# Performance work log

Hardware: AMD Instinct MI355X
Metric: run time of the kernel (lower is better)

The kernel has to match this reference:

```python
import jax, jax.numpy as jnp
import numpy as np

B, S, D_MODEL = 2, 2048, 512
N_HEADS, D_KV = 8, 64
NUM_BUCKETS, MAX_DISTANCE = 32, 128


def _relative_position_bucket(relative_position, num_buckets=NUM_BUCKETS, max_distance=MAX_DISTANCE):
    # bidirectional (is_decoder=False) bucketing, exactly as HF T5
    num_buckets = num_buckets // 2
    buckets = (relative_position > 0).astype(jnp.int32) * num_buckets
    rel = jnp.abs(relative_position)
    max_exact = num_buckets // 2
    is_small = rel < max_exact
    rel_f = jnp.maximum(rel, 1).astype(jnp.float32)
    val_if_large = max_exact + (
        jnp.log(rel_f / max_exact) / np.log(max_distance / max_exact) * (num_buckets - max_exact)
    ).astype(jnp.int32)
    val_if_large = jnp.minimum(val_if_large, num_buckets - 1)
    return buckets + jnp.where(is_small, rel, val_if_large)


def _compute_bias(rel_bias_emb, q_len, k_len):
    ctx = jnp.arange(q_len)[:, None]          # [q,1]
    mem = jnp.arange(k_len)[None, :]          # [1,k]
    buckets = _relative_position_bucket(mem - ctx)        # [q,k] int32
    bias = rel_bias_emb[buckets]                           # [q,k,H]
    return jnp.transpose(bias, (2, 0, 1))[None]            # [1,H,q,k]


def setup_inputs() -> dict:
    key = jax.random.key(0)
    ks = jax.random.split(key, 6)
    sc = 1.0 / np.sqrt(D_MODEL)
    return {
        "hidden_states": jax.random.normal(ks[0], (B, S, D_MODEL), jnp.float32),
        "Wq": jax.random.normal(ks[1], (D_MODEL, N_HEADS * D_KV), jnp.float32) * sc,
        "Wk": jax.random.normal(ks[2], (D_MODEL, N_HEADS * D_KV), jnp.float32) * sc,
        "Wv": jax.random.normal(ks[3], (D_MODEL, N_HEADS * D_KV), jnp.float32) * sc,
        "Wo": jax.random.normal(ks[4], (N_HEADS * D_KV, D_MODEL), jnp.float32) * sc,
        "rel_bias_emb": jax.random.normal(ks[5], (NUM_BUCKETS, N_HEADS), jnp.float32),
    }


def reference(hidden_states, Wq, Wk, Wv, Wo, rel_bias_emb):
    b, s, _ = hidden_states.shape

    def proj(W):  # [b,s,D] @ [D,H*Dk] -> [b,H,s,Dk]
        return (hidden_states @ W).reshape(b, s, N_HEADS, D_KV).transpose(0, 2, 1, 3)

    q = proj(Wq)
    k = proj(Wk)
    v = proj(Wv)

    # T5 attention: NO 1/sqrt(d) scaling
    scores = jnp.einsum("bhqd,bhkd->bhqk", q, k)
    position_bias = _compute_bias(rel_bias_emb, s, s)      # [1,H,s,s]
    scores = scores + position_bias
    attn = jax.nn.softmax(scores.astype(jnp.float32), axis=-1).astype(scores.dtype)
    # dropout p=0.0 in eval mode -> identity
    out = jnp.einsum("bhqk,bhkd->bhqd", attn, v)           # [b,H,s,Dk]
    out = out.transpose(0, 2, 1, 3).reshape(b, s, N_HEADS * D_KV)
    attn_output = out @ Wo                                  # [b,s,D]
    return attn_output, position_bias
```

## Files before the change

kernel.cpp:

```cpp
#include <hip/hip_runtime.h>

typedef __attribute__((ext_vector_type(8))) short short8;
typedef __attribute__((ext_vector_type(4))) float f32x4;
typedef __attribute__((ext_vector_type(16))) float f32x16;
typedef __attribute__((ext_vector_type(4))) float float4v;
typedef __attribute__((ext_vector_type(8))) float f32x8;
typedef __attribute__((ext_vector_type(4))) unsigned short us4;
typedef __attribute__((ext_vector_type(8))) unsigned short us8v;
typedef __attribute__((ext_vector_type(4))) unsigned int uint4v;

#define DEVI __device__ __forceinline__
#define MFMA16(a,b,c) __builtin_amdgcn_mfma_f32_16x16x32_bf16((a),(b),(c),0,0,0)
#define MFMA32(a,b,c) __builtin_amdgcn_mfma_f32_32x32x16_bf16((a),(b),(c),0,0,0)

DEVI unsigned short f2bf(float x) {
    unsigned u = __builtin_bit_cast(unsigned, x);
    u += 0x7FFFu + ((u >> 16) & 1u);
    return (unsigned short)(u >> 16);
}
DEVI float bf2f(unsigned short b) {
    return __builtin_bit_cast(float, ((unsigned)b) << 16);
}
DEVI unsigned cvt_pk_bf16(float lo, float hi) {
    unsigned r;
    asm("v_cvt_pk_bf16_f32 %0, %1, %2" : "=v"(r) : "v"(lo), "v"(hi));
    return r;
}

__global__ __launch_bounds__(256) void k_prep_hidden(const float* __restrict__ hid,
                                                     unsigned short* __restrict__ hh,
                                                     unsigned short* __restrict__ hl) {
    __shared__ float tile[64][65];
    const int bid = blockIdx.x;
    const int rt = bid >> 3, ct = bid & 7;
    const int t = threadIdx.x;
    const int r = t >> 2, cc = (t & 3) << 4;
    const float* sp = hid + (long)(rt * 64 + r) * 512 + ct * 64 + cc;
    #pragma unroll
    for (int j = 0; j < 16; j += 4) {
        float4v v = *reinterpret_cast<const float4v*>(sp + j);
        tile[r][cc + j + 0] = v[0];
        tile[r][cc + j + 1] = v[1];
        tile[r][cc + j + 2] = v[2];
        tile[r][cc + j + 3] = v[3];
    }
    __syncthreads();
    #pragma unroll
    for (int s = 0; s < 2; ++s) {
        int slot = t * 2 + s;
        int lane = slot & 63, i = (slot >> 6) & 3, ktl = slot >> 8;
        int ri = i * 16 + (lane & 15);
        int kc = ktl * 32 + (lane >> 4) * 8;
        us8v hv, lv;
        #pragma unroll
        for (int j = 0; j < 8; ++j) {
            float x = tile[ri][kc + j];
            unsigned short hb = f2bf(x);
            hv[j] = hb; lv[j] = f2bf(x - bf2f(hb));
        }
        long o = ((long)(rt * 16 + ct * 2 + ktl) * 4 + i) * 512 + lane * 8;
        *reinterpret_cast<us8v*>(hh + o) = hv;
        *reinterpret_cast<us8v*>(hl + o) = lv;
    }
}

__global__ __launch_bounds__(256) void k_prep_w(const float* __restrict__ wq, const float* __restrict__ wk,
                                                const float* __restrict__ wvp, const float* __restrict__ wo,
                                                unsigned short* __restrict__ wqthi, unsigned short* __restrict__ wqtlo,
                                                unsigned short* __restrict__ wkthi, unsigned short* __restrict__ wktlo,
                                                unsigned short* __restrict__ wvt, unsigned short* __restrict__ wot) {
    __shared__ float tile[64][65];
    const int bid = blockIdx.x;
    const int mat = bid >> 6, t6 = bid & 63;
    const int tr = t6 >> 3, tc = t6 & 7;
    const float* src = mat == 0 ? wq : mat == 1 ? wk : mat == 2 ? wvp : wo;
    const int t = threadIdx.x;
    const int r = t >> 2, cc = (t & 3) << 4;
    const float* sp = src + (long)(tr * 64 + r) * 512 + tc * 64 + cc;
    #pragma unroll
    for (int j = 0; j < 16; j += 4) {
        float4v v = *reinterpret_cast<const float4v*>(sp + j);
        tile[r][cc + j + 0] = v[0];
        tile[r][cc + j + 1] = v[1];
        tile[r][cc + j + 2] = v[2];
        tile[r][cc + j + 3] = v[3];
    }
    __syncthreads();
    us8v h0, h1, l0, l1;
    #pragma unroll
    for (int j = 0; j < 8; ++j) {
        float x = tile[cc + j][r];
        unsigned short hb = f2bf(x);
        h0[j] = hb; l0[j] = f2bf(x - bf2f(hb));
        float y = tile[cc + 8 + j][r];
        unsigned short hb2 = f2bf(y);
        h1[j] = hb2; l1[j] = f2bf(y - bf2f(hb2));
    }
    const int jj = r >> 4, li = r & 15;
    const int kt = (tr * 64 + cc) >> 5;
    const int g0 = (cc >> 3) & 3;
    const long bse = ((long)((tc * 16 + kt) * 4 + jj)) * 512;
    const long o0 = bse + (g0 * 16 + li) * 8;
    const long o1 = bse + ((g0 + 1) * 16 + li) * 8;
    if (mat <= 1) {
        unsigned short* oh = mat ? wkthi : wqthi;
        unsigned short* ol = mat ? wktlo : wqtlo;
        *reinterpret_cast<us8v*>(oh + o0) = h0;
        *reinterpret_cast<us8v*>(oh + o1) = h1;
        *reinterpret_cast<us8v*>(ol + o0) = l0;
        *reinterpret_cast<us8v*>(ol + o1) = l1;
    } else {
        unsigned short* oh = mat == 2 ? wvt : wot;
        *reinterpret_cast<us8v*>(oh + o0) = h0;
        *reinterpret_cast<us8v*>(oh + o1) = h1;
    }
}

DEVI int bucket_large(int a) {
    if (a < 12) return 8;
    if (a < 16) return 9;
    if (a < 23) return 10;
    if (a < 32) return 11;
    if (a < 46) return 12;
    if (a < 64) return 13;
    if (a < 91) return 14;
    return 15;
}
__global__ __launch_bounds__(256) void k_prep_bias(const float* __restrict__ emb, float* __restrict__ biasT) {
    int t = blockIdx.x * 256 + threadIdx.x;
    if (t >= 8 * 4095) return;
    int h = t / 4095;
    int idx = t - h * 4095;
    int rel = idx - 2047;
    int a = rel < 0 ? -rel : rel;
    int bucket = (rel > 0 ? 16 : 0) + (a < 8 ? a : bucket_large(a));
    biasT[h * 4096 + idx] = emb[bucket * 8 + h];
}

__global__ __launch_bounds__(256) void k_proj(const unsigned short* __restrict__ hh,
                                              const unsigned short* __restrict__ hl,
                                              const unsigned short* __restrict__ wqthi, const unsigned short* __restrict__ wqtlo,
                                              const unsigned short* __restrict__ wkthi, const unsigned short* __restrict__ wktlo,
                                              const unsigned short* __restrict__ wvt,
                                              unsigned short* __restrict__ q_hi, unsigned short* __restrict__ q_lo,
                                              unsigned short* __restrict__ ktiles,
                                              unsigned short* __restrict__ vtiles) {
    const int wgid = (blockIdx.x & 7) * 48 + (blockIdx.x >> 3);
    const int nt = wgid % 12, mt = wgid / 12;
    const int sec = nt >> 2;
    const bool isv = (sec == 2);
    const int tid = threadIdx.x, wv = tid >> 6, lane = tid & 63;
    const int wr = wv >> 1, wc = wv & 1;
    const int g = lane >> 4, li = lane & 15;
    const int m0 = mt * 128 + wr * 64;
    const int n0 = (nt & 3) * 128 + wc * 64;
    const unsigned short* bh_ = (sec == 0) ? wqthi : (sec == 1) ? wkthi : wvt;
    const unsigned short* bl_ = (sec == 0) ? wqtlo : wktlo;
    const int rt2 = m0 >> 6;
    const int ntile = n0 >> 6;

    f32x4 zf = {0.f, 0.f, 0.f, 0.f};
    f32x4 acc[4][4];
    #pragma unroll
    for (int i = 0; i < 4; ++i)
        #pragma unroll
        for (int j = 0; j < 4; ++j) acc[i][j] = zf;

    for (int ks = 0; ks < 512; ks += 32) {
        const int kt = ks >> 5;
        const long abase = ((long)(rt2 * 16 + kt) * 4) * 512 + lane * 8;
        const long bbase = ((long)(ntile * 16 + kt) * 4) * 512 + lane * 8;
        short8 ah[4], al[4], bhf[4], blf[4];
        #pragma unroll
        for (int i = 0; i < 4; ++i) {
            ah[i] = *reinterpret_cast<const short8*>(hh + abase + i * 512);
            if (!isv) al[i] = *reinterpret_cast<const short8*>(hl + abase + i * 512);
            bhf[i] = *reinterpret_cast<const short8*>(bh_ + bbase + i * 512);
            if (!isv) blf[i] = *reinterpret_cast<const short8*>(bl_ + bbase + i * 512);
        }
        #pragma unroll
        for (int i = 0; i < 4; ++i)
            #pragma unroll
            for (int j = 0; j < 4; ++j) {
                acc[i][j] = MFMA16(ah[i], bhf[j], acc[i][j]);
                if (!isv) {
                    acc[i][j] = MFMA16(ah[i], blf[j], acc[i][j]);
                    acc[i][j] = MFMA16(al[i], bhf[j], acc[i][j]);
                }
            }
    }

    if (sec == 0) {
        #pragma unroll
        for (int i = 0; i < 4; ++i) {
            int rowb = m0 + i * 16 + g * 4;
            #pragma unroll
            for (int j = 0; j < 4; ++j) {
                int col = n0 + j * 16 + li;
                #pragma unroll
                for (int r = 0; r < 4; ++r) {
                    float x = acc[i][j][r];
                    unsigned short hb = f2bf(x);
                    long o = (long)(rowb + r) * 512 + col;
                    q_hi[o] = hb;
                    q_lo[o] = f2bf(x - bf2f(hb));
                }
            }
        }
    } else if (sec == 1) {
        #pragma unroll
        for (int i = 0; i < 4; ++i) {
            int rowb = m0 + i * 16 + g * 4;
            #pragma unroll
            for (int j = 0; j < 4; ++j) {
                int col = n0 + j * 16 + li;
                int h2 = col >> 6, d = col & 63;
                int ds2 = d >> 4, j2 = d & 7, lhalf = (d >> 3) & 1;
                #pragma unroll
                for (int r = 0; r < 4; ++r) {
                    int srow = rowb + r;
                    int bloc = srow >> 11, k = srow & 2047;
                    long base = (long)((bloc * 8 + h2) * 64 + (k >> 5)) * 4096
                              + (((k & 31) | (lhalf << 5)) * 8 + j2);
                    float x = acc[i][j][r];
                    unsigned short hb = f2bf(x);
                    ktiles[base + ds2 * 512] = hb;
                    ktiles[base + (4 + ds2) * 512] = f2bf(x - bf2f(hb));
                }
            }
        }
    } else {
        #pragma unroll
        for (int i = 0; i < 4; ++i) {
            int rowb = m0 + i * 16 + g * 4;
            int bloc = rowb >> 11, k = rowb & 2047;
            int kt = k >> 5, t = (k >> 4) & 1, lhalf = (k >> 3) & 1, j0 = k & 7;
            #pragma unroll
            for (int j = 0; j < 4; ++j) {
                int col = n0 + j * 16 + li;
                int h2 = col >> 6, d = col & 63;
                int dblk = d >> 5;
                us4 w;
                #pragma unroll
                for (int r = 0; r < 4; ++r) w[r] = f2bf(acc[i][j][r]);
                long off2 = (long)((bloc * 8 + h2) * 64 + kt) * 2048
                          + (dblk * 2 + t) * 512 + (((d & 31) | (lhalf << 5)) * 8 + j0);
                *reinterpret_cast<us4*>(vtiles + off2) = w;
            }
        }
    }
}

__global__ __launch_bounds__(128) void k_attn(const unsigned short* __restrict__ qhi,
                                              const unsigned short* __restrict__ qlo,
                                              const unsigned short* __restrict__ ktiles,
                                              const unsigned short* __restrict__ vtiles,
                                              const float* __restrict__ biasT,
                                              unsigned short* __restrict__ ctx,
                                              float* __restrict__ outb) {
    __shared__ float lb[2080];
    __shared__ float mrg[64][34];
    const int xcd = blockIdx.x & 7, lidx = blockIdx.x >> 3;
    const int bh = ((lidx >> 6) << 3) | xcd;
    const int qt = lidx & 63;
    const int b = bh >> 3, h = bh & 7;
    const int tid = threadIdx.x;
    const int kh = tid >> 6, lane = tid & 63;
    const int ql_ = lane & 31, hi = lane >> 5;
    const int q0 = qt * 32;

    for (int i = tid; i < 2080; i += 128) lb[i] = biasT[h * 4096 + (2016 - q0) + i];
    __syncthreads();

    const int q = q0 + ql_;
    const long rowQ = (long)(b * 2048 + q) * 512 + h * 64 + hi * 8;
    short8 qfh[4], qfl[4];
    #pragma unroll
    for (int ds = 0; ds < 4; ++ds) {
        qfh[ds] = *reinterpret_cast<const short8*>(qhi + rowQ + ds * 16);
        qfl[ds] = *reinterpret_cast<const short8*>(qlo + rowQ + ds * 16);
    }
    const int kbeg = kh * 1024;
    const unsigned short* ktb = ktiles + ((long)bh * 64 + (kbeg >> 5)) * 4096;
    const unsigned short* vtb = vtiles + ((long)bh * 64 + (kbeg >> 5)) * 2048;

    f32x16 o0, o1;
    #pragma unroll
    for (int i = 0; i < 16; ++i) { o0[i] = 0.f; o1[i] = 0.f; }
    float m_run = -__builtin_inff(), l_run = 0.f;

    short8 kAh[4], kAl[4], kBh[4], kBl[4], vA[4], vB[4];
    #pragma unroll
    for (int ds = 0; ds < 4; ++ds) {
        kAh[ds] = *reinterpret_cast<const short8*>(ktb + ds * 512 + lane * 8);
        kAl[ds] = *reinterpret_cast<const short8*>(ktb + (4 + ds) * 512 + lane * 8);
    }
    #pragma unroll
    for (int i = 0; i < 4; ++i)
        vA[i] = *reinterpret_cast<const short8*>(vtb + i * 512 + lane * 8);

    auto step = [&](short8 (&ckh)[4], short8 (&ckl)[4], short8 (&cv)[4],
                    short8 (&nkh)[4], short8 (&nkl)[4], short8 (&nv)[4], int it) {
        f32x16 ssA, ssB;
        #pragma unroll
        for (int i = 0; i < 16; ++i) { ssA[i] = 0.f; ssB[i] = 0.f; }
        __builtin_amdgcn_s_setprio(1);
        #pragma unroll
        for (int ds = 0; ds < 4; ++ds) {
            ssA = MFMA32(ckh[ds], qfh[ds], ssA);
            ssB = MFMA32(ckh[ds], qfl[ds], ssB);
        }
        #pragma unroll
        for (int ds = 0; ds < 4; ++ds)
            ssA = MFMA32(ckl[ds], qfh[ds], ssA);
        __builtin_amdgcn_s_setprio(0);
        const long ko = (it + 1 < 32) ? (long)(it + 1) * 4096 : (long)it * 4096;
        const long vo = (it + 1 < 32) ? (long)(it + 1) * 2048 : (long)it * 2048;
        #pragma unroll
        for (int ds = 0; ds < 4; ++ds) {
            nkh[ds] = *reinterpret_cast<const short8*>(ktb + ko + ds * 512 + lane * 8);
            nkl[ds] = *reinterpret_cast<const short8*>(ktb + ko + (4 + ds) * 512 + lane * 8);
        }
        #pragma unroll
        for (int i = 0; i < 4; ++i)
            nv[i] = *reinterpret_cast<const short8*>(vtb + vo + i * 512 + lane * 8);
        const int k0 = kbeg + it * 32;
        const int ib = k0 - ql_ + 31 + 4 * hi;
        float s[16];
        #pragma unroll
        for (int r = 0; r < 16; ++r)
            s[r] = (ssA[r] + ssB[r]) + lb[ib + (r & 3) + 8 * (r >> 2)];
        float t0 = fmaxf(s[0], s[1]), t1 = fmaxf(s[2], s[3]), t2 = fmaxf(s[4], s[5]), t3 = fmaxf(s[6], s[7]);
        float t4 = fmaxf(s[8], s[9]), t5 = fmaxf(s[10], s[11]), t6 = fmaxf(s[12], s[13]), t7 = fmaxf(s[14], s[15]);
        float u0 = fmaxf(t0, t1), u1 = fmaxf(t2, t3), u2 = fmaxf(t4, t5), u3 = fmaxf(t6, t7);
        float mx = fmaxf(fmaxf(u0, u1), fmaxf(u2, u3));
        mx = fmaxf(mx, __shfl_xor(mx, 32));
        bool grown = mx > m_run;
        float mnew = fmaxf(m_run, mx);
        float scale = __expf(m_run - mnew);
        float p[16];
        #pragma unroll
        for (int r = 0; r < 16; ++r) p[r] = __expf(s[r] - mnew);
        unsigned W[8];
        float ps[8];
        #pragma unroll
        for (int r2 = 0; r2 < 8; ++r2) {
            unsigned w = cvt_pk_bf16(p[2 * r2], p[2 * r2 + 1]);
            W[r2] = w;
            float plo = __builtin_bit_cast(float, w << 16);
            float phi = __builtin_bit_cast(float, w & 0xFFFF0000u);
            ps[r2] = plo + phi;
        }
        float psum = ((ps[0] + ps[1]) + (ps[2] + ps[3])) + ((ps[4] + ps[5]) + (ps[6] + ps[7]));
        l_run = l_run * scale + psum;
        m_run = mnew;
        if (__any(grown)) {
            #pragma unroll
            for (int i = 0; i < 16; ++i) { o0[i] *= scale; o1[i] *= scale; }
        }
        unsigned Sw[8];
        #pragma unroll
        for (int r2 = 0; r2 < 8; ++r2) Sw[r2] = __shfl_xor(W[r2], 32);
        __builtin_amdgcn_s_setprio(1);
        #pragma unroll
        for (int t = 0; t < 2; ++t) {
            uint4v bw;
            bw[0] = hi ? Sw[4 * t + 2] : W[4 * t + 0];
            bw[1] = hi ? Sw[4 * t + 3] : W[4 * t + 1];
            bw[2] = hi ? W[4 * t + 2] : Sw[4 * t + 0];
            bw[3] = hi ? W[4 * t + 3] : Sw[4 * t + 1];
            short8 pf = __builtin_bit_cast(short8, bw);
            o0 = MFMA32(cv[t], pf, o0);
            o1 = MFMA32(cv[2 + t], pf, o1);
        }
        __builtin_amdgcn_s_setprio(0);
    };

    for (int it2 = 0; it2 < 32; it2 += 2) {
        step(kAh, kAl, vA, kBh, kBl, vB, it2);
        step(kBh, kBl, vB, kAh, kAl, vA, it2 + 1);
    }

    if (kh == 1) {
        float* mp = &mrg[lane][0];
        mp[0] = m_run; mp[1] = l_run;
        #pragma unroll
        for (int i = 0; i < 16; ++i) { mp[2 + i] = o0[i]; mp[18 + i] = o1[i]; }
    }
    __syncthreads();
    if (kh == 0) {
        const float* mp = &mrg[lane][0];
        float m2 = mp[0], l2 = mp[1];
        float ms = fmaxf(m_run, m2);
        float a1 = __expf(m_run - ms);
        float a2 = __expf(m2 - ms);
        float lt = l_run * a1 + l2 * a2;
        lt += __shfl_xor(lt, 32);
        float inv = 1.0f / lt;
        const int rt = b * 32 + (q >> 6), ii = (q >> 4) & 3, li2 = q & 15;
        const long baseA = ((long)(rt * 16 + 2 * h) * 4 + ii) * 512 + li2 * 8 + 4 * hi;
        #pragma unroll
        for (int a = 0; a < 4; ++a) {
            us4 w0, w1;
            #pragma unroll
            for (int c = 0; c < 4; ++c) {
                w0[c] = f2bf((o0[4 * a + c] * a1 + mp[2 + 4 * a + c] * a2) * inv);
                w1[c] = f2bf((o1[4 * a + c] * a1 + mp[18 + 4 * a + c] * a2) * inv);
            }
            *reinterpret_cast<us4*>(ctx + baseA + a * 128) = w0;
            *reinterpret_cast<us4*>(ctx + baseA + 2048 + a * 128) = w1;
        }
    }

    if (b == 0) {
        float* ob = outb + ((long)h * 2048 + q0) * 2048;
        const float* bsrc = biasT + h * 4096 + 2047 - q0;
        #pragma unroll 4
        for (int c = 0; c < 64; ++c) {
            int chunk = c * 128 + tid;
            int r = chunk >> 8;
            int k8 = (chunk & 255) * 8;
            const float* src = bsrc + (k8 - r);
            f32x8 w;
            #pragma unroll
            for (int i = 0; i < 8; ++i) w[i] = src[i];
            *reinterpret_cast<f32x8*>(ob + (long)r * 2048 + k8) = w;
        }
    }
}

__global__ __launch_bounds__(256) void k_oproj(const unsigned short* __restrict__ ctx,
                                               const unsigned short* __restrict__ wot,
                                               float* __restrict__ outp) {
    const int wgid = blockIdx.x;
    const int nt = wgid & 3, mt = wgid >> 2;
    const int tid = threadIdx.x, wv = tid >> 6, lane = tid & 63;
    const int wr = wv >> 1, wc = wv & 1;
    const int g = lane >> 4, li = lane & 15;
    const int m0 = mt * 128 + wr * 64;
    const int n0 = nt * 128 + wc * 64;
    const int rt2 = m0 >> 6, ntile = n0 >> 6;

    f32x4 zf = {0.f, 0.f, 0.f, 0.f};
    f32x4 acc[4][4];
    #pragma unroll
    for (int i = 0; i < 4; ++i)
        #pragma unroll
        for (int j = 0; j < 4; ++j) acc[i][j] = zf;

    for (int ks = 0; ks < 512; ks += 32) {
        const int kt = ks >> 5;
        const long abase = (long)(rt2 * 16 + kt) * 2048 + lane * 8;
        const long bbase = (long)(ntile * 16 + kt) * 2048 + lane * 8;
        short8 af[4], bf[4];
        #pragma unroll
        for (int i = 0; i < 4; ++i) {
            af[i] = *reinterpret_cast<const short8*>(ctx + abase + i * 512);
            bf[i] = *reinterpret_cast<const short8*>(wot + bbase + i * 512);
        }
        #pragma unroll
        for (int i = 0; i < 4; ++i)
            #pragma unroll
            for (int j = 0; j < 4; ++j)
                acc[i][j] = MFMA16(af[i], bf[j], acc[i][j]);
    }
    #pragma unroll
    for (int i = 0; i < 4; ++i) {
        int rowb = m0 + i * 16 + g * 4;
        #pragma unroll
        for (int j = 0; j < 4; ++j) {
            int col = n0 + j * 16 + li;
            #pragma unroll
            for (int r = 0; r < 4; ++r)
                outp[(long)(rowb + r) * 512 + col] = acc[i][j][r];
        }
    }
}

extern "C" void kernel_launch(void* const* d_in, const int* in_sizes, int n_in,
                              void* d_out, int out_size, void* d_ws, size_t ws_size,
                              hipStream_t stream) {
    const float* hidden = (const float*)d_in[0];
    const float* Wq = (const float*)d_in[1];
    const float* Wk = (const float*)d_in[2];
    const float* Wv = (const float*)d_in[3];
    const float* Wo = (const float*)d_in[4];
    const float* emb = (const float*)d_in[5];
    float* out = (float*)d_out;

    char* ws = (char*)d_ws;
    size_t off = 0;
    auto alloc = [&](size_t bytes) { char* p = ws + off; off += (bytes + 255) & ~(size_t)255; return p; };

    unsigned short* hid_hi = (unsigned short*)alloc(4096ull * 512 * 2);
    unsigned short* hid_lo = (unsigned short*)alloc(4096ull * 512 * 2);
    unsigned short* wqthi  = (unsigned short*)alloc(512ull * 512 * 2);
    unsigned short* wqtlo  = (unsigned short*)alloc(512ull * 512 * 2);
    unsigned short* wkthi  = (unsigned short*)alloc(512ull * 512 * 2);
    unsigned short* wktlo  = (unsigned short*)alloc(512ull * 512 * 2);
    unsigned short* wvt    = (unsigned short*)alloc(512ull * 512 * 2);
    unsigned short* wot    = (unsigned short*)alloc(512ull * 512 * 2);
    float*          biasT  = (float*)alloc(8ull * 4096 * 4);
    unsigned short* q_hi   = (unsigned short*)alloc(4096ull * 512 * 2);
    unsigned short* q_lo   = (unsigned short*)alloc(4096ull * 512 * 2);
    unsigned short* ktiles = (unsigned short*)alloc(16ull * 64 * 8 * 512 * 2);
    unsigned short* vtiles = (unsigned short*)alloc(16ull * 64 * 4 * 512 * 2);
    unsigned short* ctx    = (unsigned short*)alloc(4096ull * 512 * 2);

    k_prep_hidden<<<512, 256, 0, stream>>>(hidden, hid_hi, hid_lo);
    k_prep_w<<<256, 256, 0, stream>>>(Wq, Wk, Wv, Wo, wqthi, wqtlo, wkthi, wktlo, wvt, wot);
    k_prep_bias<<<128, 256, 0, stream>>>(emb, biasT);
    k_proj<<<384, 256, 0, stream>>>(hid_hi, hid_lo, wqthi, wqtlo, wkthi, wktlo, wvt,
                                    q_hi, q_lo, ktiles, vtiles);
    k_attn<<<1024, 128, 0, stream>>>(q_hi, q_lo, ktiles, vtiles, biasT, ctx, out + 2097152);
    k_oproj<<<128, 256, 0, stream>>>(ctx, wot, out);
}
```

Baseline: 127.6 us.

## Split attention key range across four waves per block with LDS merge

The attention kernel now launches 256 threads per block and splits the 2048 keys across four waves of 512 keys each instead of two waves of 1024. The three extra partial softmax states are merged through shared memory by wave 0. The row-sum is now taken from fp32 probabilities rather than bf16-rounded ones, and the max reduction is reshaped. The goal is more parallelism per query tile and shorter serial loops, at the cost of more LDS, a longer merge step and possibly lower occupancy.

Result: slower. 148.8 us (+16.6%).

```diff
diff --git a/kernel.cpp b/kernel.cpp
--- a/kernel.cpp
+++ b/kernel.cpp
@@ -251,7 +251,7 @@
     }
 }
 
-__global__ __launch_bounds__(128) void k_attn(const unsigned short* __restrict__ qhi,
+__global__ __launch_bounds__(256) void k_attn(const unsigned short* __restrict__ qhi,
                                               const unsigned short* __restrict__ qlo,
                                               const unsigned short* __restrict__ ktiles,
                                               const unsigned short* __restrict__ vtiles,
@@ -259,17 +259,17 @@
                                               unsigned short* __restrict__ ctx,
                                               float* __restrict__ outb) {
     __shared__ float lb[2080];
-    __shared__ float mrg[64][34];
+    __shared__ float mrg[3][64][34];
     const int xcd = blockIdx.x & 7, lidx = blockIdx.x >> 3;
     const int bh = ((lidx >> 6) << 3) | xcd;
     const int qt = lidx & 63;
     const int b = bh >> 3, h = bh & 7;
     const int tid = threadIdx.x;
-    const int kh = tid >> 6, lane = tid & 63;
+    const int kq = tid >> 6, lane = tid & 63;
     const int ql_ = lane & 31, hi = lane >> 5;
     const int q0 = qt * 32;
 
-    for (int i = tid; i < 2080; i += 128) lb[i] = biasT[h * 4096 + (2016 - q0) + i];
+    for (int i = tid; i < 2080; i += 256) lb[i] = biasT[h * 4096 + (2016 - q0) + i];
     __syncthreads();
 
     const int q = q0 + ql_;
@@ -280,7 +280,7 @@
         qfh[ds] = *reinterpret_cast<const short8*>(qhi + rowQ + ds * 16);
         qfl[ds] = *reinterpret_cast<const short8*>(qlo + rowQ + ds * 16);
     }
-    const int kbeg = kh * 1024;
+    const int kbeg = kq * 512;
     const unsigned short* ktb = ktiles + ((long)bh * 64 + (kbeg >> 5)) * 4096;
     const unsigned short* vtb = vtiles + ((long)bh * 64 + (kbeg >> 5)) * 2048;
 
@@ -314,8 +314,8 @@
         for (int ds = 0; ds < 4; ++ds)
             ssA = MFMA32(ckl[ds], qfh[ds], ssA);
         __builtin_amdgcn_s_setprio(0);
-        const long ko = (it + 1 < 32) ? (long)(it + 1) * 4096 : (long)it * 4096;
-        const long vo = (it + 1 < 32) ? (long)(it + 1) * 2048 : (long)it * 2048;
+        const long ko = (it + 1 < 16) ? (long)(it + 1) * 4096 : (long)it * 4096;
+        const long vo = (it + 1 < 16) ? (long)(it + 1) * 2048 : (long)it * 2048;
         #pragma unroll
         for (int ds = 0; ds < 4; ++ds) {
             nkh[ds] = *reinterpret_cast<const short8*>(ktb + ko + ds * 512 + lane * 8);
@@ -330,10 +330,14 @@
         #pragma unroll
         for (int r = 0; r < 16; ++r)
             s[r] = (ssA[r] + ssB[r]) + lb[ib + (r & 3) + 8 * (r >> 2)];
-        float t0 = fmaxf(s[0], s[1]), t1 = fmaxf(s[2], s[3]), t2 = fmaxf(s[4], s[5]), t3 = fmaxf(s[6], s[7]);
-        float t4 = fmaxf(s[8], s[9]), t5 = fmaxf(s[10], s[11]), t6 = fmaxf(s[12], s[13]), t7 = fmaxf(s[14], s[15]);
-        float u0 = fmaxf(t0, t1), u1 = fmaxf(t2, t3), u2 = fmaxf(t4, t5), u3 = fmaxf(t6, t7);
-        float mx = fmaxf(fmaxf(u0, u1), fmaxf(u2, u3));
+        float a0 = fmaxf(fmaxf(s[0], s[1]), s[2]);
+        float a1b = fmaxf(fmaxf(s[3], s[4]), s[5]);
+        float a2b = fmaxf(fmaxf(s[6], s[7]), s[8]);
+        float a3 = fmaxf(fmaxf(s[9], s[10]), s[11]);
+        float a4 = fmaxf(fmaxf(s[12], s[13]), s[14]);
+        float b0 = fmaxf(fmaxf(a0, a1b), a2b);
+        float b1 = fmaxf(fmaxf(a3, a4), s[15]);
+        float mx = fmaxf(b0, b1);
         mx = fmaxf(mx, __shfl_xor(mx, 32));
         bool grown = mx > m_run;
         float mnew = fmaxf(m_run, mx);
@@ -341,17 +345,12 @@
         float p[16];
         #pragma unroll
         for (int r = 0; r < 16; ++r) p[r] = __expf(s[r] - mnew);
+        float psum = (((p[0] + p[1]) + (p[2] + p[3])) + ((p[4] + p[5]) + (p[6] + p[7])))
+                   + (((p[8] + p[9]) + (p[10] + p[11])) + ((p[12] + p[13]) + (p[14] + p[15])));
         unsigned W[8];
-        float ps[8];
-        #pragma unroll
-        for (int r2 = 0; r2 < 8; ++r2) {
-            unsigned w = cvt_pk_bf16(p[2 * r2], p[2 * r2 + 1]);
-            W[r2] = w;
-            float plo = __builtin_bit_cast(float, w << 16);
-            float phi = __builtin_bit_cast(float, w & 0xFFFF0000u);
-            ps[r2] = plo + phi;
-        }
-        float psum = ((ps[0] + ps[1]) + (ps[2] + ps[3])) + ((ps[4] + ps[5]) + (ps[6] + ps[7]));
+        #pragma unroll
+        for (int r2 = 0; r2 < 8; ++r2)
+            W[r2] = cvt_pk_bf16(p[2 * r2], p[2 * r2 + 1]);
         l_run = l_run * scale + psum;
         m_run = mnew;
         if (__any(grown)) {
@@ -376,26 +375,35 @@
         __builtin_amdgcn_s_setprio(0);
     };
 
-    for (int it2 = 0; it2 < 32; it2 += 2) {
+    for (int it2 = 0; it2 < 16; it2 += 2) {
         step(kAh, kAl, vA, kBh, kBl, vB, it2);
         step(kBh, kBl, vB, kAh, kAl, vA, it2 + 1);
     }
 
-    if (kh == 1) {
-        float* mp = &mrg[lane][0];
+    if (kq != 0) {
+        float* mp = &mrg[kq - 1][lane][0];
         mp[0] = m_run; mp[1] = l_run;
         #pragma unroll
         for (int i = 0; i < 16; ++i) { mp[2 + i] = o0[i]; mp[18 + i] = o1[i]; }
     }
     __syncthreads();
-    if (kh == 0) {
-        const float* mp = &mrg[lane][0];
-        float m2 = mp[0], l2 = mp[1];
-        float ms = fmaxf(m_run, m2);
-        float a1 = __expf(m_run - ms);
-        float a2 = __expf(m2 - ms);
-        float lt = l_run * a1 + l2 * a2;
-        lt += __shfl_xor(lt, 32);
+    if (kq == 0) {
+        #pragma unroll
+        for (int j = 0; j < 3; ++j) {
+            const float* mp = &mrg[j][lane][0];
+            float m2 = mp[0], l2 = mp[1];
+            float ms = fmaxf(m_run, m2);
+            float a1 = __expf(m_run - ms);
+            float a2 = __expf(m2 - ms);
+            l_run = l_run * a1 + l2 * a2;
+            m_run = ms;
+            #pragma unroll
+            for (int i = 0; i < 16; ++i) {
+                o0[i] = o0[i] * a1 + mp[2 + i] * a2;
+                o1[i] = o1[i] * a1 + mp[18 + i] * a2;
+            }
+        }
+        float lt = l_run + __shfl_xor(l_run, 32);
         float inv = 1.0f / lt;
         const int rt = b * 32 + (q >> 6), ii = (q >> 4) & 3, li2 = q & 15;
         const long baseA = ((long)(rt * 16 + 2 * h) * 4 + ii) * 512 + li2 * 8 + 4 * hi;
@@ -404,8 +412,8 @@
             us4 w0, w1;
             #pragma unroll
             for (int c = 0; c < 4; ++c) {
-                w0[c] = f2bf((o0[4 * a + c] * a1 + mp[2 + 4 * a + c] * a2) * inv);
-                w1[c] = f2bf((o1[4 * a + c] * a1 + mp[18 + 4 * a + c] * a2) * inv);
+                w0[c] = f2bf(o0[4 * a + c] * inv);
+                w1[c] = f2bf(o1[4 * a + c] * inv);
             }
             *reinterpret_cast<us4*>(ctx + baseA + a * 128) = w0;
             *reinterpret_cast<us4*>(ctx + baseA + 2048 + a * 128) = w1;
@@ -416,8 +424,8 @@
         float* ob = outb + ((long)h * 2048 + q0) * 2048;
         const float* bsrc = biasT + h * 4096 + 2047 - q0;
         #pragma unroll 4
-        for (int c = 0; c < 64; ++c) {
-            int chunk = c * 128 + tid;
+        for (int c = 0; c < 32; ++c) {
+            int chunk = c * 256 + tid;
             int r = chunk >> 8;
             int k8 = (chunk & 255) * 8;
             const float* src = bsrc + (k8 - r);
@@ -512,6 +520,6 @@
     k_prep_bias<<<128, 256, 0, stream>>>(emb, biasT);
     k_proj<<<384, 256, 0, stream>>>(hid_hi, hid_lo, wqthi, wqtlo, wkthi, wktlo, wvt,
                                     q_hi, q_lo, ktiles, vtiles);
-    k_attn<<<1024, 128, 0, stream>>>(q_hi, q_lo, ktiles, vtiles, biasT, ctx, out + 2097152);
+    k_attn<<<1024, 256, 0, stream>>>(q_hi, q_lo, ktiles, vtiles, biasT, ctx, out + 2097152);
     k_oproj<<<128, 256, 0, stream>>>(ctx, wot, out);
 }
```
